# Optimization experiments

Hardware: AMD Instinct MI355X
Metric: run time of the kernel (lower is better)

## Reference

```python
import jax, jax.numpy as jnp
import numpy as np

B = 16          # number of variable-length sequences
T = 131072      # total tokens (sum of lengths)
E = 2048        # embedding_size
O = 1024        # output_size


def setup_inputs() -> dict:
    key = jax.random.key(0)
    kx, kw, kb = jax.random.split(key, 3)
    # random partition of T into B positive segment lengths
    rs = np.random.RandomState(0)
    cuts = np.sort(rs.choice(np.arange(1, T), size=B - 1, replace=False))
    lengths = np.diff(np.concatenate([[0], cuts, [T]])).astype(np.int64)
    x = jax.random.normal(kx, (T, E), dtype=jnp.float32)
    W = jax.random.normal(kw, (E, O), dtype=jnp.float32) * 0.02  # Linear weight (stored transposed)
    b = jnp.zeros((O,), dtype=jnp.float32)                        # Linear bias
    return {"x": x, "W": W, "b": b, "lengths": jnp.asarray(lengths)}


def reference(x, W, b, lengths):
    # Fused segmented mean over ragged sequences, then linear projection.
    T_ = x.shape[0]
    B_ = lengths.shape[0]
    offsets = jnp.cumsum(lengths)                                   # [B] exclusive-end offsets
    seg_ids = jnp.searchsorted(offsets, jnp.arange(T_), side="right")  # [T] segment id per row
    sums = jax.ops.segment_sum(x, seg_ids, num_segments=B_)        # [B, E]
    means = sums / lengths[:, None].astype(x.dtype)                # per-segment mean
    return means @ W + b                                           # [B, O]
```

## Files before the change

kernel.cpp:

```cpp
#include <hip/hip_runtime.h>


#define E_DIM 2048
#define O_DIM 1024
#define R_CHUNK 64
#define S_SPLIT 8

typedef float v4f __attribute__((ext_vector_type(4)));

__global__ __launch_bounds__(256, 8) void seg_partial(const float* __restrict__ x,
                                                      const int* __restrict__ lengths,
                                                      int Bn,
                                                      float* __restrict__ partial) {
    const int g = blockIdx.x;
    int off = 0, cb = 0, r0 = 0, r1 = 0, found = 0;
    for (int i = 0; i < Bn; ++i) {
        const int l  = lengths[i];
        const int nc = (l + R_CHUNK - 1) / R_CHUNK;
        if (g < cb + nc) {
            r0 = off + (g - cb) * R_CHUNK;
            r1 = min(r0 + R_CHUNK, off + l);
            found = 1;
            break;
        }
        off += l; cb += nc;
    }
    if (!found) return;

    const int tx = threadIdx.x;
    v4f a0 = {0.f, 0.f, 0.f, 0.f};
    v4f a1 = {0.f, 0.f, 0.f, 0.f};
    const v4f* p = (const v4f*)(x + (size_t)r0 * E_DIM + tx * 4);
#pragma unroll 4
    for (int r = r0; r < r1; ++r) {
        v4f v0 = __builtin_nontemporal_load(p);
        v4f v1 = __builtin_nontemporal_load(p + 256);
        a0 += v0;
        a1 += v1;
        p += E_DIM / 4;
    }
    v4f* dst = (v4f*)(partial + (size_t)g * E_DIM + tx * 4);
    dst[0]   = a0;
    dst[256] = a1;
}

__global__ __launch_bounds__(256) void reduce_p2(const float* __restrict__ partial,
                                                 const int* __restrict__ lengths,
                                                 int Bn,
                                                 float* __restrict__ p2) {
    const int b = blockIdx.y;
    const int s = blockIdx.z;
    int cb = 0;
    for (int i = 0; i < b; ++i) cb += (lengths[i] + R_CHUNK - 1) / R_CHUNK;
    const int nch = (lengths[b] + R_CHUNK - 1) / R_CHUNK;
    const int c0 = (nch * s) / S_SPLIT;
    const int c1 = (nch * (s + 1)) / S_SPLIT;

    const int col = blockIdx.x * 1024 + threadIdx.x * 4;
    v4f acc = {0.f, 0.f, 0.f, 0.f};
    const v4f* p = (const v4f*)(partial + (size_t)(cb + c0) * E_DIM + col);
#pragma unroll 8
    for (int c = c0; c < c1; ++c) {
        acc += *p;
        p += E_DIM / 4;
    }
    *(v4f*)(p2 + ((size_t)(b * S_SPLIT + s)) * E_DIM + col) = acc;
}

__global__ __launch_bounds__(512) void gemm_out(const float* __restrict__ p2,
                                                const float* __restrict__ W,
                                                const float* __restrict__ bias,
                                                const int* __restrict__ lengths,
                                                float* __restrict__ out) {
    const int b      = blockIdx.y;
    const int tx     = threadIdx.x;
    const int olocal = tx & 63;
    const int eg     = tx >> 6;
    const int o      = blockIdx.x * 64 + olocal;

    __shared__ float m_lds[E_DIM];
    __shared__ float red[S_SPLIT][64];

    {
        const float inv = 1.0f / (float)lengths[b];
        const int col = tx * 4;
        const v4f* ps = (const v4f*)(p2 + (size_t)b * S_SPLIT * E_DIM + col);
        v4f m = {0.f, 0.f, 0.f, 0.f};
#pragma unroll
        for (int s = 0; s < S_SPLIT; ++s)
            m += ps[s * (E_DIM / 4)];
        m *= inv;
        *(v4f*)(m_lds + col) = m;
    }
    __syncthreads();

    float a0 = 0.f, a1 = 0.f, a2 = 0.f, a3 = 0.f;
    const float* wp = W + (size_t)(eg * 256) * O_DIM + o;
    const float* mp = m_lds + eg * 256;
#pragma unroll 8
    for (int i = 0; i < 256; i += 4) {
        a0 += mp[i + 0] * wp[(size_t)(i + 0) * O_DIM];
        a1 += mp[i + 1] * wp[(size_t)(i + 1) * O_DIM];
        a2 += mp[i + 2] * wp[(size_t)(i + 2) * O_DIM];
        a3 += mp[i + 3] * wp[(size_t)(i + 3) * O_DIM];
    }
    red[eg][olocal] = (a0 + a1) + (a2 + a3);
    __syncthreads();

    if (tx < 64) {
        float r = bias[blockIdx.x * 64 + tx];
#pragma unroll
        for (int s = 0; s < S_SPLIT; ++s) r += red[s][tx];
        out[b * O_DIM + blockIdx.x * 64 + tx] = r;
    }
}

extern "C" void kernel_launch(void* const* d_in, const int* in_sizes, int n_in,
                              void* d_out, int out_size, void* d_ws, size_t ws_size,
                              hipStream_t stream) {
    const float* x       = (const float*)d_in[0];
    const float* W       = (const float*)d_in[1];
    const float* bias    = (const float*)d_in[2];
    const int*   lengths = (const int*)d_in[3];

    const int Bn = in_sizes[3];
    const int On = in_sizes[2];
    const int En = in_sizes[1] / On;
    const int Tn = in_sizes[0] / En;
    (void)En; (void)out_size; (void)n_in; (void)ws_size;

    const int maxChunks      = (Tn + R_CHUNK - 1) / R_CHUNK;
    const int maxTotalChunks = maxChunks + Bn;

    float* partial = (float*)d_ws;
    float* p2      = partial + (size_t)maxTotalChunks * E_DIM;

    seg_partial<<<maxTotalChunks, 256, 0, stream>>>(x, lengths, Bn, partial);

    dim3 g2(E_DIM / 1024, Bn, S_SPLIT);
    reduce_p2<<<g2, 256, 0, stream>>>(partial, lengths, Bn, p2);

    dim3 g3(On / 64, Bn);
    gemm_out<<<g3, 512, 0, stream>>>(p2, W, bias, lengths, (float*)d_out);
}
```

Before: 201.3 us.

## Align chunks to global rows, raise reduce split, tile batch in GEMM

```diff
diff --git a/kernel.cpp b/kernel.cpp
--- a/kernel.cpp
+++ b/kernel.cpp
@@ -3,67 +3,78 @@
 
 #define E_DIM 2048
 #define O_DIM 1024
-#define R_CHUNK 64
-#define S_SPLIT 8
+#define RCH 64
+#define S_SPLIT 16
+#define B_TILE 4
 
 typedef float v4f __attribute__((ext_vector_type(4)));
 
 __global__ __launch_bounds__(256, 8) void seg_partial(const float* __restrict__ x,
                                                       const int* __restrict__ lengths,
-                                                      int Bn,
-                                                      float* __restrict__ partial) {
-    const int g = blockIdx.x;
-    int off = 0, cb = 0, r0 = 0, r1 = 0, found = 0;
-    for (int i = 0; i < Bn; ++i) {
-        const int l  = lengths[i];
-        const int nc = (l + R_CHUNK - 1) / R_CHUNK;
-        if (g < cb + nc) {
-            r0 = off + (g - cb) * R_CHUNK;
-            r1 = min(r0 + R_CHUNK, off + l);
-            found = 1;
-            break;
-        }
-        off += l; cb += nc;
-    }
-    if (!found) return;
+                                                      int Bn, int Tn,
+                                                      float* __restrict__ mainp,
+                                                      float* __restrict__ extrap) {
+    const int g  = blockIdx.x;
+    const int r0 = g * RCH;
+    const int rEnd = min(r0 + RCH, Tn);
+
+    int b = 0, segEnd = lengths[0];
+    while (segEnd <= r0) { ++b; segEnd += lengths[b]; }
 
     const int tx = threadIdx.x;
+    const v4f* p = (const v4f*)(x + (size_t)r0 * E_DIM + tx * 4);
     v4f a0 = {0.f, 0.f, 0.f, 0.f};
     v4f a1 = {0.f, 0.f, 0.f, 0.f};
-    const v4f* p = (const v4f*)(x + (size_t)r0 * E_DIM + tx * 4);
+    int r = r0;
+    bool first = true;
+    while (true) {
+        const int stop = min(rEnd, segEnd);
 #pragma unroll 4
-    for (int r = r0; r < r1; ++r) {
-        v4f v0 = __builtin_nontemporal_load(p);
-        v4f v1 = __builtin_nontemporal_load(p + 256);
-        a0 += v0;
-        a1 += v1;
-        p += E_DIM / 4;
+        for (; r < stop; ++r) {
+            v4f v0 = __builtin_nontemporal_load(p);
+            v4f v1 = __builtin_nontemporal_load(p + 256);
+            a0 += v0;
+            a1 += v1;
+            p += E_DIM / 4;
+        }
+        float* dst = first ? (mainp + (size_t)g * E_DIM)
+                           : (extrap + (size_t)b * E_DIM);
+        v4f* d = (v4f*)dst + tx;
+        d[0]   = a0;
+        d[256] = a1;
+        if (r >= rEnd) break;
+        first = false;
+        ++b; segEnd += lengths[b];
+        a0 = (v4f){0.f, 0.f, 0.f, 0.f};
+        a1 = (v4f){0.f, 0.f, 0.f, 0.f};
     }
-    v4f* dst = (v4f*)(partial + (size_t)g * E_DIM + tx * 4);
-    dst[0]   = a0;
-    dst[256] = a1;
 }
 
-__global__ __launch_bounds__(256) void reduce_p2(const float* __restrict__ partial,
+__global__ __launch_bounds__(256) void reduce_p2(const float* __restrict__ mainp,
+                                                 const float* __restrict__ extrap,
                                                  const int* __restrict__ lengths,
-                                                 int Bn,
                                                  float* __restrict__ p2) {
     const int b = blockIdx.y;
     const int s = blockIdx.z;
-    int cb = 0;
-    for (int i = 0; i < b; ++i) cb += (lengths[i] + R_CHUNK - 1) / R_CHUNK;
-    const int nch = (lengths[b] + R_CHUNK - 1) / R_CHUNK;
-    const int c0 = (nch * s) / S_SPLIT;
-    const int c1 = (nch * (s + 1)) / S_SPLIT;
+    int start = 0;
+    for (int i = 0; i < b; ++i) start += lengths[i];
+    const int end = start + lengths[b];
+    const int g0 = (start + RCH - 1) / RCH;
+    const int g1 = (end - 1) / RCH;
+    const int nch = (g1 >= g0) ? (g1 - g0 + 1) : 0;
+    const int c0 = g0 + (nch * s) / S_SPLIT;
+    const int c1 = g0 + (nch * (s + 1)) / S_SPLIT;
 
     const int col = blockIdx.x * 1024 + threadIdx.x * 4;
     v4f acc = {0.f, 0.f, 0.f, 0.f};
-    const v4f* p = (const v4f*)(partial + (size_t)(cb + c0) * E_DIM + col);
+    const v4f* p = (const v4f*)(mainp + (size_t)c0 * E_DIM + col);
 #pragma unroll 8
     for (int c = c0; c < c1; ++c) {
         acc += *p;
         p += E_DIM / 4;
     }
+    if (s == 0 && (start % RCH) != 0)
+        acc += *(const v4f*)(extrap + (size_t)b * E_DIM + col);
     *(v4f*)(p2 + ((size_t)(b * S_SPLIT + s)) * E_DIM + col) = acc;
 }
 
@@ -72,46 +83,51 @@
                                                 const float* __restrict__ bias,
                                                 const int* __restrict__ lengths,
                                                 float* __restrict__ out) {
-    const int b      = blockIdx.y;
-    const int tx     = threadIdx.x;
+    const int oc = blockIdx.x;
+    const int bc = blockIdx.y;
+    const int tx = threadIdx.x;
     const int olocal = tx & 63;
     const int eg     = tx >> 6;
-    const int o      = blockIdx.x * 64 + olocal;
+    const int o      = oc * 64 + olocal;
 
-    __shared__ float m_lds[E_DIM];
-    __shared__ float red[S_SPLIT][64];
+    __shared__ float m_lds[B_TILE][E_DIM];
+    __shared__ float red[B_TILE][8][64];
 
-    {
-        const float inv = 1.0f / (float)lengths[b];
-        const int col = tx * 4;
-        const v4f* ps = (const v4f*)(p2 + (size_t)b * S_SPLIT * E_DIM + col);
+    for (int i = tx; i < B_TILE * (E_DIM / 4); i += 512) {
+        const int bb = i / (E_DIM / 4);
+        const int cv = i % (E_DIM / 4);
+        const int b  = bc * B_TILE + bb;
+        const v4f* ps = (const v4f*)(p2 + (size_t)b * S_SPLIT * E_DIM) + cv;
         v4f m = {0.f, 0.f, 0.f, 0.f};
 #pragma unroll
-        for (int s = 0; s < S_SPLIT; ++s)
-            m += ps[s * (E_DIM / 4)];
-        m *= inv;
-        *(v4f*)(m_lds + col) = m;
+        for (int s2 = 0; s2 < S_SPLIT; ++s2)
+            m += ps[s2 * (E_DIM / 4)];
+        m *= (1.0f / (float)lengths[b]);
+        ((v4f*)m_lds[bb])[cv] = m;
     }
     __syncthreads();
 
-    float a0 = 0.f, a1 = 0.f, a2 = 0.f, a3 = 0.f;
+    float acc[B_TILE] = {0.f, 0.f, 0.f, 0.f};
     const float* wp = W + (size_t)(eg * 256) * O_DIM + o;
-    const float* mp = m_lds + eg * 256;
-#pragma unroll 8
-    for (int i = 0; i < 256; i += 4) {
-        a0 += mp[i + 0] * wp[(size_t)(i + 0) * O_DIM];
-        a1 += mp[i + 1] * wp[(size_t)(i + 1) * O_DIM];
-        a2 += mp[i + 2] * wp[(size_t)(i + 2) * O_DIM];
-        a3 += mp[i + 3] * wp[(size_t)(i + 3) * O_DIM];
+    const float* mp = &m_lds[0][eg * 256];
+#pragma unroll 4
+    for (int i = 0; i < 256; ++i) {
+        const float w = wp[(size_t)i * O_DIM];
+#pragma unroll
+        for (int bb = 0; bb < B_TILE; ++bb)
+            acc[bb] += mp[bb * E_DIM + i] * w;
     }
-    red[eg][olocal] = (a0 + a1) + (a2 + a3);
+#pragma unroll
+    for (int bb = 0; bb < B_TILE; ++bb)
+        red[bb][eg][olocal] = acc[bb];
     __syncthreads();
 
-    if (tx < 64) {
-        float r = bias[blockIdx.x * 64 + tx];
+    if (tx < B_TILE * 64) {
+        const int bb = tx >> 6, ol = tx & 63;
+        float r = bias[oc * 64 + ol];
 #pragma unroll
-        for (int s = 0; s < S_SPLIT; ++s) r += red[s][tx];
-        out[b * O_DIM + blockIdx.x * 64 + tx] = r;
+        for (int e2 = 0; e2 < 8; ++e2) r += red[bb][e2][ol];
+        out[(size_t)(bc * B_TILE + bb) * O_DIM + oc * 64 + ol] = r;
     }
 }
 
@@ -129,17 +145,17 @@
     const int Tn = in_sizes[0] / En;
     (void)En; (void)out_size; (void)n_in; (void)ws_size;
 
-    const int maxChunks      = (Tn + R_CHUNK - 1) / R_CHUNK;
-    const int maxTotalChunks = maxChunks + Bn;
+    const int nChunks = (Tn + RCH - 1) / RCH;
 
-    float* partial = (float*)d_ws;
-    float* p2      = partial + (size_t)maxTotalChunks * E_DIM;
+    float* mainp = (float*)d_ws;
+    float* extrap = mainp + (size_t)nChunks * E_DIM;
+    float* p2     = extrap + (size_t)Bn * E_DIM;
 
-    seg_partial<<<maxTotalChunks, 256, 0, stream>>>(x, lengths, Bn, partial);
+    seg_partial<<<nChunks, 256, 0, stream>>>(x, lengths, Bn, Tn, mainp, extrap);
 
     dim3 g2(E_DIM / 1024, Bn, S_SPLIT);
-    reduce_p2<<<g2, 256, 0, stream>>>(partial, lengths, Bn, p2);
+    reduce_p2<<<g2, 256, 0, stream>>>(mainp, extrap, lengths, p2);
 
-    dim3 g3(On / 64, Bn);
+    dim3 g3(On / 64, Bn / B_TILE);
     gemm_out<<<g3, 512, 0, stream>>>(p2, W, bias, lengths, (float*)d_out);
 }
```

New measurement: 213.4 us. +6.0%, slower.

## Use segment-agnostic aligned 64-row chunks and handle segment edges in reduce

Applied to the files above, without the earlier changes.

```diff
diff --git a/kernel.cpp b/kernel.cpp
--- a/kernel.cpp
+++ b/kernel.cpp
@@ -3,67 +3,72 @@
 
 #define E_DIM 2048
 #define O_DIM 1024
-#define R_CHUNK 64
+#define RCH 64
 #define S_SPLIT 8
 
 typedef float v4f __attribute__((ext_vector_type(4)));
 
-__global__ __launch_bounds__(256, 8) void seg_partial(const float* __restrict__ x,
-                                                      const int* __restrict__ lengths,
-                                                      int Bn,
-                                                      float* __restrict__ partial) {
-    const int g = blockIdx.x;
-    int off = 0, cb = 0, r0 = 0, r1 = 0, found = 0;
-    for (int i = 0; i < Bn; ++i) {
-        const int l  = lengths[i];
-        const int nc = (l + R_CHUNK - 1) / R_CHUNK;
-        if (g < cb + nc) {
-            r0 = off + (g - cb) * R_CHUNK;
-            r1 = min(r0 + R_CHUNK, off + l);
-            found = 1;
-            break;
-        }
-        off += l; cb += nc;
-    }
-    if (!found) return;
-
+__global__ __launch_bounds__(256, 8) void sum64(const float* __restrict__ x,
+                                                float* __restrict__ mainp) {
+    const int g  = blockIdx.x;
     const int tx = threadIdx.x;
+    const v4f* p = (const v4f*)(x + (size_t)g * (RCH * E_DIM)) + tx;
     v4f a0 = {0.f, 0.f, 0.f, 0.f};
     v4f a1 = {0.f, 0.f, 0.f, 0.f};
-    const v4f* p = (const v4f*)(x + (size_t)r0 * E_DIM + tx * 4);
 #pragma unroll 4
-    for (int r = r0; r < r1; ++r) {
-        v4f v0 = __builtin_nontemporal_load(p);
-        v4f v1 = __builtin_nontemporal_load(p + 256);
-        a0 += v0;
-        a1 += v1;
+    for (int r = 0; r < RCH; ++r) {
+        a0 += __builtin_nontemporal_load(p);
+        a1 += __builtin_nontemporal_load(p + 256);
         p += E_DIM / 4;
     }
-    v4f* dst = (v4f*)(partial + (size_t)g * E_DIM + tx * 4);
-    dst[0]   = a0;
-    dst[256] = a1;
+    v4f* d = (v4f*)(mainp + (size_t)g * E_DIM) + tx;
+    d[0]   = a0;
+    d[256] = a1;
 }
 
-__global__ __launch_bounds__(256) void reduce_p2(const float* __restrict__ partial,
+__global__ __launch_bounds__(256) void reduce_p2(const float* __restrict__ mainp,
+                                                 const float* __restrict__ x,
                                                  const int* __restrict__ lengths,
-                                                 int Bn,
                                                  float* __restrict__ p2) {
     const int b = blockIdx.y;
     const int s = blockIdx.z;
-    int cb = 0;
-    for (int i = 0; i < b; ++i) cb += (lengths[i] + R_CHUNK - 1) / R_CHUNK;
-    const int nch = (lengths[b] + R_CHUNK - 1) / R_CHUNK;
-    const int c0 = (nch * s) / S_SPLIT;
-    const int c1 = (nch * (s + 1)) / S_SPLIT;
+    int start = 0;
+    for (int i = 0; i < b; ++i) start += lengths[i];
+    const int end = start + lengths[b];
+
+    const int cs = (start + RCH - 1) / RCH;
+    const int ce = end / RCH;
+    int headLo, headHi, tailLo, tailHi, c0, c1;
+    if (ce < cs) {
+        headLo = start; headHi = end;
+        tailLo = 0;     tailHi = 0;
+        c0 = 0;         c1 = 0;
+    } else {
+        headLo = start;    headHi = cs * RCH;
+        tailLo = ce * RCH; tailHi = end;
+        const int n = ce - cs;
+        c0 = cs + (n * s) / S_SPLIT;
+        c1 = cs + (n * (s + 1)) / S_SPLIT;
+    }
+    const int hn = headHi - headLo;
+    const int h0 = headLo + (hn * s) / S_SPLIT;
+    const int h1 = headLo + (hn * (s + 1)) / S_SPLIT;
+    const int tn = tailHi - tailLo;
+    const int t0 = tailLo + (tn * s) / S_SPLIT;
+    const int t1 = tailLo + (tn * (s + 1)) / S_SPLIT;
 
     const int col = blockIdx.x * 1024 + threadIdx.x * 4;
     v4f acc = {0.f, 0.f, 0.f, 0.f};
-    const v4f* p = (const v4f*)(partial + (size_t)(cb + c0) * E_DIM + col);
-#pragma unroll 8
+    for (int r = h0; r < h1; ++r)
+        acc += *(const v4f*)(x + (size_t)r * E_DIM + col);
+    const v4f* p = (const v4f*)(mainp + (size_t)c0 * E_DIM + col);
+#pragma unroll 4
     for (int c = c0; c < c1; ++c) {
         acc += *p;
         p += E_DIM / 4;
     }
+    for (int r = t0; r < t1; ++r)
+        acc += *(const v4f*)(x + (size_t)r * E_DIM + col);
     *(v4f*)(p2 + ((size_t)(b * S_SPLIT + s)) * E_DIM + col) = acc;
 }
 
@@ -129,16 +134,15 @@
     const int Tn = in_sizes[0] / En;
     (void)En; (void)out_size; (void)n_in; (void)ws_size;
 
-    const int maxChunks      = (Tn + R_CHUNK - 1) / R_CHUNK;
-    const int maxTotalChunks = maxChunks + Bn;
+    const int nChunks = Tn / RCH;
 
-    float* partial = (float*)d_ws;
-    float* p2      = partial + (size_t)maxTotalChunks * E_DIM;
+    float* mainp = (float*)d_ws;
+    float* p2    = mainp + (size_t)nChunks * E_DIM;
 
-    seg_partial<<<maxTotalChunks, 256, 0, stream>>>(x, lengths, Bn, partial);
+    sum64<<<nChunks, 256, 0, stream>>>(x, mainp);
 
     dim3 g2(E_DIM / 1024, Bn, S_SPLIT);
-    reduce_p2<<<g2, 256, 0, stream>>>(partial, lengths, Bn, p2);
+    reduce_p2<<<g2, 256, 0, stream>>>(mainp, x, lengths, p2);
 
     dim3 g3(On / 64, Bn);
     gemm_out<<<g3, 512, 0, stream>>>(p2, W, bias, lengths, (float*)d_out);
```

Result: no change. 198.1 us (-1.6%).
